# Kernel tuning notes

Hardware: AMD Instinct MI355X
Metric: run time of the kernel (lower is better)

The kernel has to match this reference:

```python
import jax, jax.numpy as jnp
import numpy as np

B = 32768; E = 9; RANK = 50; K = 2
N_ENT = 40943; N_REL = 22
LOSS_COEF = 0.01; NOISE_EPS = 0.01
EPS = float(np.finfo(np.float64).eps)


def setup_inputs():
    key = jax.random.key(0)
    ks = jax.random.split(key, 12)
    q0 = jax.random.randint(ks[0], (B,), 0, N_ENT)
    q1 = jax.random.randint(ks[1], (B,), 0, N_REL)
    q2 = jax.random.randint(ks[2], (B,), 0, N_ENT)
    queries = jnp.stack([q0, q1, q2], axis=1)
    t2 = jax.random.randint(ks[3], (B,), 0, N_ENT)
    these_queries = jnp.stack([q0, q1, t2], axis=1)
    D = E * RANK
    entity = jax.random.normal(ks[4], (N_ENT, D), jnp.float32) / D
    rel = jax.random.normal(ks[5], (N_REL, 2 * D), jnp.float32) / (2 * D)
    rel_diag = 2.0 * jax.random.uniform(ks[6], (N_REL, D), jnp.float32) - 1.0
    bh = jnp.zeros((N_ENT, 1), jnp.float32)
    bt = jnp.zeros((N_ENT, 1), jnp.float32)
    c_param = jnp.ones((N_REL, 1), jnp.float32)
    cnn_w = 0.1 * jax.random.normal(ks[7], (1, 1, 5, 5), jnp.float32)
    cnn_b = jnp.zeros((1,), jnp.float32)
    h2e_w = 0.05 * jax.random.normal(ks[8], (E, 128), jnp.float32)
    h2e_b = jnp.zeros((E,), jnp.float32)
    cnnn_w = 0.1 * jax.random.normal(ks[9], (1, 1, 5, 5), jnp.float32)
    cnnn_b = jnp.zeros((1,), jnp.float32)
    h2en_w = 0.05 * jax.random.normal(ks[10], (E, 128), jnp.float32)
    h2en_b = jnp.zeros((E,), jnp.float32)
    noise = jax.random.normal(ks[11], (B, E), jnp.float32)
    return {"queries": queries, "these_queries": these_queries, "entity": entity,
            "rel": rel, "rel_diag": rel_diag, "bh": bh, "bt": bt, "c_param": c_param,
            "cnn_w": cnn_w, "cnn_b": cnn_b, "h2e_w": h2e_w, "h2e_b": h2e_b,
            "cnnn_w": cnnn_w, "cnnn_b": cnnn_b, "h2en_w": h2en_w, "h2en_b": h2en_b,
            "noise": noise}


def _conv(x, w, b):
    # x: [B,1,27,50], w: [1,1,5,5], stride 3, VALID -> [B,1,8,16]
    y = jax.lax.conv_general_dilated(x, w, (3, 3), 'VALID',
                                     dimension_numbers=('NCHW', 'OIHW', 'NCHW'))
    return y + b.reshape(1, -1, 1, 1)


def _phi(z):
    # standard normal CDF
    return 0.5 * (1.0 + jax.lax.erf(z * 0.7071067811865476))


def _givens_rot(r, x):
    # r, x: [B,E,RANK]; rotate consecutive dim-pairs by normalized (cos,sin) from r
    shp = r.shape[:-1] + (RANK // 2, 2)
    r2 = r.reshape(shp); x2 = x.reshape(shp)
    nrm = jnp.maximum(jnp.linalg.norm(r2, axis=-1, keepdims=True), 1e-15)
    cs = r2 / nrm
    o0 = cs[..., 0] * x2[..., 0] - cs[..., 1] * x2[..., 1]
    o1 = cs[..., 1] * x2[..., 0] + cs[..., 0] * x2[..., 1]
    return jnp.stack([o0, o1], axis=-1).reshape(r.shape)


def _cv_squared(v):
    return jnp.var(v, ddof=1) / (jnp.mean(v) ** 2 + 1e-10)


def reference(queries, these_queries, entity, rel, rel_diag, bh, bt, c_param,
              cnn_w, cnn_b, h2e_w, h2e_b, cnnn_w, cnnn_b, h2en_w, h2en_b, noise):
    q0, q1 = queries[:, 0], queries[:, 1]
    t2 = these_queries[:, 2]
    head = entity[q0]                  # [B, E*RANK]
    rel_q = rel[q1]                    # [B, 2*E*RANK]
    rel_diag_q = rel_diag[q1]          # [B, E*RANK]
    c = jax.nn.softplus(c_param[q1])   # [B, 1]
    lhs_b = bh[q0]                     # [B, 1]
    rhs_b = bt[t2]                     # [B, 1]
    rhs_e = entity[t2]                 # [B, E*RANK]

    # ---- noisy top-k gating ----
    x = jnp.concatenate([head, rel_q], axis=-1).reshape(-1, 1, 3 * E, RANK)
    feat = _conv(x, cnn_w, cnn_b).reshape(-1, 128)
    clean = feat @ h2e_w.T + h2e_b                      # [B, E]
    feat_n = _conv(x, cnnn_w, cnnn_b).reshape(-1, 128)
    raw_std = feat_n @ h2en_w.T + h2en_b
    std = jax.nn.softplus(raw_std) + NOISE_EPS
    noisy = clean + noise * std                         # train=1

    top_logits, top_idx = jax.lax.top_k(noisy, K + 1)
    tk_logits = top_logits[:, :K]
    tk_idx = top_idx[:, :K]
    tk_gates = jax.nn.softmax(tk_logits, axis=-1)
    gates = jnp.zeros_like(noisy).at[jnp.arange(noisy.shape[0])[:, None], tk_idx].set(tk_gates)

    thr_in = top_logits[:, K:K + 1]
    thr_out = top_logits[:, K - 1:K]
    is_in = noisy > thr_in
    prob = jnp.where(is_in, _phi((clean - thr_in) / std), _phi((clean - thr_out) / std))
    load = prob.sum(0)
    importance = gates.sum(0)
    loss = LOSS_COEF * (_cv_squared(importance) + _cv_squared(load))

    # ---- experts, computed densely over [B, E, RANK] then masked-combined ----
    head_r = head.reshape(-1, E, RANK)
    rhs_r = rhs_e.reshape(-1, E, RANK)
    rel_r = rel_q.reshape(-1, E, 2 * RANK)
    rd_r = rel_diag_q.reshape(-1, E, RANK)
    lhs = _givens_rot(rd_r, head_r) + rel_r[..., :RANK]
    dist2 = jnp.sum((lhs - rhs_r) ** 2, axis=-1)        # [B, E]
    score = lhs_b + rhs_b - c * dist2                   # [B, E]

    # SparseDispatcher.combine with use_log_sum_exp=True, multiply_by_gates=False
    mask = gates > 0
    s = jnp.sum(jnp.where(mask, jnp.exp(score), 0.0), axis=1, keepdims=True)
    y = jnp.log(jnp.where(s == 0, EPS, s))              # [B, 1]
    return y, loss
```

## Files before the change

### kernel.cpp

```cpp
#include <hip/hip_runtime.h>
#include <math.h>

#define BATCH 32768
#define NE 9
#define RANK 50
#define DIM 450
#define REL_DIM 900
#define N_REL 22
#define EPSV 2.2204460492503131e-16f
#define SPB 4

#define LANE_FENCE() asm volatile("" ::: "memory")

__device__ __forceinline__ float softplusf(float x) {
    return (x > 20.f) ? x : log1pf(expf(x));
}
__device__ __forceinline__ float phif(float z) {
    return 0.5f * (1.f + erff(z * 0.70710678118654752f));
}

__global__ __launch_bounds__(64) void k_pre(
    const float* __restrict__ rel, const float* __restrict__ rel_diag,
    const float* __restrict__ c_param,
    const float* __restrict__ cnn_w, const float* __restrict__ cnn_b,
    const float* __restrict__ cnnn_w, const float* __restrict__ cnnn_b,
    const float* __restrict__ h2e_w, const float* __restrict__ h2en_w,
    float* __restrict__ cs_tab, float* __restrict__ pre_out, float* __restrict__ c_soft)
{
    const int r = blockIdx.x;
    const int l = threadIdx.x;
    __shared__ float rl[REL_DIM];
    __shared__ float fA[80], fB[80];

    const float* relp = rel + (size_t)r * REL_DIM;
    for (int i = l; i < REL_DIM; i += 64) rl[i] = relp[i];
    __syncthreads();

    const float cb0 = cnn_b[0], cb1 = cnnn_b[0];
    for (int idx = l; idx < 80; idx += 64) {
        int o = 48 + idx;
        int oh = o >> 4, ow = o & 15;
        const float* base = rl + (oh * 3 - 9) * RANK + ow * 3;
        float a0 = cb0, a1 = cb1;
#pragma unroll
        for (int i = 0; i < 5; ++i)
#pragma unroll
            for (int j = 0; j < 5; ++j) {
                float v = base[i * RANK + j];
                a0 = fmaf(v, cnn_w[i * 5 + j], a0);
                a1 = fmaf(v, cnnn_w[i * 5 + j], a1);
            }
        fA[idx] = a0; fB[idx] = a1;
    }
    __syncthreads();

    if (l < 18) {
        int e = (l < 9) ? l : (l - 9);
        const float* w = ((l < 9) ? (h2e_w + e * 128) : (h2en_w + e * 128)) + 48;
        const float* f = (l < 9) ? fA : fB;
        float acc = 0.f;
#pragma unroll 8
        for (int t = 0; t < 80; ++t) acc = fmaf(f[t], w[t], acc);
        pre_out[r * 18 + l] = acc;
    }
    if (l == 63) c_soft[r] = softplusf(c_param[r]);

    const float2* rd2 = (const float2*)(rel_diag + (size_t)r * DIM);
    float2* cs2 = (float2*)(cs_tab + (size_t)r * DIM);
    for (int u = l; u < 225; u += 64) {
        float2 v = rd2[u];
        float nrm = fmaxf(sqrtf(v.x * v.x + v.y * v.y), 1e-15f);
        cs2[u] = make_float2(v.x / nrm, v.y / nrm);
    }
}

__global__ __launch_bounds__(64) void k_main(
    const int* __restrict__ queries, const int* __restrict__ these_queries,
    const float* __restrict__ entity, const float* __restrict__ rel,
    const float* __restrict__ bh, const float* __restrict__ bt,
    const float* __restrict__ cnn_w, const float* __restrict__ cnn_b,
    const float* __restrict__ h2e_w, const float* __restrict__ h2e_b,
    const float* __restrict__ cnnn_w, const float* __restrict__ cnnn_b,
    const float* __restrict__ h2en_w, const float* __restrict__ h2en_b,
    const float* __restrict__ noise,
    const float* __restrict__ cs_tab, const float* __restrict__ pre_out,
    const float* __restrict__ c_soft,
    float* __restrict__ y_out, float* __restrict__ ws_rows)
{
    const int l = threadIdx.x;

    __shared__ __align__(16) float  xs[552];
    __shared__ __align__(16) float2 fs[51];
    float2* xs2 = (float2*)xs;

    const int base = blockIdx.x * SPB;

    int q0 = queries[base * 3 + 0];
    int q1 = queries[base * 3 + 1];
    int t2 = these_queries[base * 3 + 2];
    float2 h2[4];
    {
        const float2* hp2 = (const float2*)(entity + (size_t)q0 * DIM);
#pragma unroll
        for (int k = 0; k < 4; ++k) { int i = l + 64 * k; if (i < 225) h2[k] = hp2[i]; }
    }
    float2 rr2 = make_float2(0.f, 0.f);
    if (l < 50) rr2 = ((const float2*)(rel + (size_t)q1 * REL_DIM))[l];
    float nz    = (l < NE) ? noise[(size_t)base * NE + l] : 0.f;
    float pre_v = (l < 18) ? pre_out[q1 * 18 + l] : 0.f;
    float bhv = bh[q0], btv = bt[t2], csv = c_soft[q1];

#pragma unroll
    for (int s = 0; s < SPB; ++s) {
        const int b = base + s;
        const int   cq1 = q1, ct2 = t2;
        const float cnz = nz, cpre = pre_v, cbh = bhv, cbt = btv, ccs = csv;

#pragma unroll
        for (int k = 0; k < 4; ++k) { int i = l + 64 * k; if (i < 225) xs2[i] = h2[k]; }
        if (l < 50) xs2[225 + l] = rr2;
        LANE_FENCE();

        if (s + 1 < SPB) {
            const int nb = b + 1;
            q0 = queries[nb * 3 + 0];
            q1 = queries[nb * 3 + 1];
            t2 = these_queries[nb * 3 + 2];
            const float2* hp2 = (const float2*)(entity + (size_t)q0 * DIM);
#pragma unroll
            for (int k = 0; k < 4; ++k) { int i = l + 64 * k; if (i < 225) h2[k] = hp2[i]; }
            rr2 = make_float2(0.f, 0.f);
            if (l < 50) rr2 = ((const float2*)(rel + (size_t)q1 * REL_DIM))[l];
            nz    = (l < NE) ? noise[(size_t)nb * NE + l] : 0.f;
            pre_v = (l < 18) ? pre_out[q1 * 18 + l] : 0.f;
            bhv = bh[q0]; btv = bt[t2]; csv = c_soft[q1];
        }

        if (l < 48) {
            int oh = l >> 4, ow = l & 15;
            const float* bp = xs + (oh * 3) * RANK + ow * 3;
            float a0 = cnn_b[0], a1 = cnnn_b[0];
#pragma unroll
            for (int i = 0; i < 5; ++i)
#pragma unroll
                for (int j = 0; j < 5; ++j) {
                    float v = bp[i * RANK + j];
                    a0 = fmaf(v, cnn_w[i * 5 + j], a0);
                    a1 = fmaf(v, cnnn_w[i * 5 + j], a1);
                }
            fs[l + (l >> 4)] = make_float2(a0, a1);
        }
        LANE_FENCE();

        float acc = 0.f;
        if (l < 54) {
            int chunk = l / 18, j = l - chunk * 18;
            int e = (j < 9) ? j : (j - 9);
            const float* wrow = ((j < 9) ? (h2e_w + e * 128) : (h2en_w + e * 128)) + chunk * 16;
            int fbase = chunk * 17;
            if (j < 9) {
#pragma unroll
                for (int k = 0; k < 16; ++k) acc = fmaf(fs[fbase + k].x, wrow[k], acc);
            } else {
#pragma unroll
                for (int k = 0; k < 16; ++k) acc = fmaf(fs[fbase + k].y, wrow[k], acc);
            }
        }
        float pA = __shfl_down(acc, 18);
        float pB = __shfl_down(acc, 36);
        float tot = acc + pA + pB;

        float myv = 0.f;
        if (l < 9)       myv = tot + cpre + h2e_b[l];
        else if (l < 18) myv = softplusf(tot + cpre + h2en_b[l - 9]) + 0.01f;
        float sd = __shfl_down(myv, 9);
        float nv = fmaf(cnz, sd, myv);

        int i0 = -1, i1 = -1;
        float v0 = -__builtin_huge_valf(), v1 = v0, v2 = v0;
#pragma unroll
        for (int e = 0; e < NE; ++e) {
            float v = __shfl(nv, e);
            if (v > v0)      { v2 = v1; v1 = v0; i1 = i0; v0 = v; i0 = e; }
            else if (v > v1) { v2 = v1; v1 = v; i1 = e; }
            else if (v > v2) { v2 = v; }
        }
        float e1 = expf(v1 - v0);
        float inv = 1.f / (1.f + e1);
        float g0 = inv, g1 = e1 * inv;
        float thr_in = v2, thr_out = v1;

        int srcl = (l >= 9 && l < 18) ? (l - 9) : 0;
        float cl_e = __shfl(myv, srcl);
        float nv_e = __shfl(nv, srcl);

        float contrib = 0.f;
        bool act = (l < 25) || (l >= 32 && l < 57);
        if (act) {
            int sel = (l >= 32) ? 1 : 0;
            int p = l - 32 * sel;
            int e = sel ? i1 : i0;
            int u = e * 25 + p;
            float2 cs = *(const float2*)(cs_tab + (size_t)cq1 * DIM + 2 * u);
            float2 rl = *(const float2*)(rel + (size_t)cq1 * REL_DIM + e * 100 + 2 * p);
            float2 rh = *(const float2*)(entity + (size_t)ct2 * DIM + 2 * u);
            float2 x  = xs2[u];
            float o0 = cs.x * x.x - cs.y * x.y + rl.x;
            float o1 = cs.y * x.x + cs.x * x.y + rl.y;
            float d0 = o0 - rh.x, d1 = o1 - rh.y;
            contrib = fmaf(d0, d0, d1 * d1);
        }

        if (l < NE) {
            float g = (l == i0) ? g0 : ((l == i1) ? g1 : 0.f);
            ws_rows[(size_t)b * 18 + l] = g;
        } else if (l < 18) {
            float thr = (nv_e > thr_in) ? thr_in : thr_out;
            ws_rows[(size_t)b * 18 + l] = phif((cl_e - thr) / myv);
        }

#pragma unroll
        for (int off = 16; off; off >>= 1) contrib += __shfl_xor(contrib, off);
        float d2b = __shfl(contrib, 32);
        if (l == 0) {
            float bsum = cbh + cbt;
            float sacc = expf(bsum - ccs * contrib) + expf(bsum - ccs * d2b);
            y_out[b] = logf((sacc == 0.f) ? EPSV : sacc);
        }
        LANE_FENCE();
    }
}

__global__ __launch_bounds__(64) void k_reduce(const float* __restrict__ ws_rows,
                                               float* __restrict__ partials)
{
    const int blk = blockIdx.x, t = threadIdx.x;
    float acc[18];
#pragma unroll
    for (int j = 0; j < 18; ++j) acc[j] = 0.f;
    const int r0 = blk * 128 + t * 2;
#pragma unroll
    for (int rr = 0; rr < 2; ++rr) {
        const float2* row = (const float2*)(ws_rows + (size_t)(r0 + rr) * 18);
#pragma unroll
        for (int j = 0; j < 9; ++j) {
            float2 v = row[j];
            acc[2 * j] += v.x; acc[2 * j + 1] += v.y;
        }
    }
#pragma unroll
    for (int j = 0; j < 18; ++j) {
        float v = acc[j];
        for (int off = 32; off; off >>= 1) v += __shfl_down(v, off);
        if (t == 0) partials[blk * 18 + j] = v;
    }
}

__global__ __launch_bounds__(64) void k_loss(const float* __restrict__ partials,
                                             float* __restrict__ out)
{
    __shared__ float sums[18];
    const int t = threadIdx.x;
    if (t < 18) {
        float s = 0.f;
        for (int p0 = 0; p0 < 256; p0 += 16) {
            float v[16];
#pragma unroll
            for (int k = 0; k < 16; ++k) v[k] = partials[(p0 + k) * 18 + t];
#pragma unroll
            for (int k = 0; k < 16; ++k) s += v[k];
        }
        sums[t] = s;
    }
    __syncthreads();
    if (t == 0) {
        float loss = 0.f;
#pragma unroll
        for (int part = 0; part < 2; ++part) {
            const float* v = sums + part * NE;
            float mean = 0.f;
            for (int i = 0; i < NE; ++i) mean += v[i];
            mean /= 9.f;
            float var = 0.f;
            for (int i = 0; i < NE; ++i) { float d = v[i] - mean; var += d * d; }
            var /= 8.f;
            loss += var / (mean * mean + 1e-10f);
        }
        out[BATCH] = 0.01f * loss;
    }
}

extern "C" void kernel_launch(void* const* d_in, const int* in_sizes, int n_in,
                              void* d_out, int out_size, void* d_ws, size_t ws_size,
                              hipStream_t stream)
{
    const int*   queries = (const int*)d_in[0];
    const int*   these   = (const int*)d_in[1];
    const float* entity  = (const float*)d_in[2];
    const float* rel     = (const float*)d_in[3];
    const float* rel_dg  = (const float*)d_in[4];
    const float* bh      = (const float*)d_in[5];
    const float* bt      = (const float*)d_in[6];
    const float* c_par   = (const float*)d_in[7];
    const float* cnn_w   = (const float*)d_in[8];
    const float* cnn_b   = (const float*)d_in[9];
    const float* h2e_w   = (const float*)d_in[10];
    const float* h2e_b   = (const float*)d_in[11];
    const float* cnnn_w  = (const float*)d_in[12];
    const float* cnnn_b  = (const float*)d_in[13];
    const float* h2en_w  = (const float*)d_in[14];
    const float* h2en_b  = (const float*)d_in[15];
    const float* noise   = (const float*)d_in[16];

    float* y  = (float*)d_out;
    float* ws = (float*)d_ws;
    float* ws_rows  = ws;
    float* partials = ws + (size_t)BATCH * 18;
    float* cs_tab   = partials + 256 * 18;
    float* pre_out  = cs_tab + N_REL * DIM;
    float* c_soft   = pre_out + N_REL * 18;

    k_pre<<<N_REL, 64, 0, stream>>>(rel, rel_dg, c_par, cnn_w, cnn_b, cnnn_w, cnnn_b,
                                    h2e_w, h2en_w, cs_tab, pre_out, c_soft);
    k_main<<<BATCH / SPB, 64, 0, stream>>>(queries, these, entity, rel, bh, bt,
                                           cnn_w, cnn_b, h2e_w, h2e_b, cnnn_w, cnnn_b,
                                           h2en_w, h2en_b, noise, cs_tab, pre_out, c_soft,
                                           y, ws_rows);
    k_reduce<<<256, 64, 0, stream>>>(ws_rows, partials);
    k_loss<<<1, 64, 0, stream>>>(partials, y);
}
```

Measured before the change: 193.7 us.

## Process one sample per block instead of four with software prefetch

Removes the four-samples-per-block loop and its software prefetch of the next sample's entity row and relation data, launching one 64-thread block per batch element. Query indices are made wave-uniform with readfirstlane so the gathered row addresses can stay in scalar registers. The aim is more independent blocks to hide gather latency through occupancy instead of in-block prefetch. The cost is four times as many blocks and more per-block setup, including repeated loads of the small weight vectors.

```diff
diff --git a/kernel.cpp b/kernel.cpp
--- a/kernel.cpp
+++ b/kernel.cpp
@@ -8,7 +8,6 @@
 #define REL_DIM 900
 #define N_REL 22
 #define EPSV 2.2204460492503131e-16f
-#define SPB 4
 
 #define LANE_FENCE() asm volatile("" ::: "memory")
 
@@ -87,17 +86,17 @@
     const float* __restrict__ c_soft,
     float* __restrict__ y_out, float* __restrict__ ws_rows)
 {
+    const int b = blockIdx.x;
     const int l = threadIdx.x;
 
     __shared__ __align__(16) float  xs[552];
     __shared__ __align__(16) float2 fs[51];
     float2* xs2 = (float2*)xs;
 
-    const int base = blockIdx.x * SPB;
-
-    int q0 = queries[base * 3 + 0];
-    int q1 = queries[base * 3 + 1];
-    int t2 = these_queries[base * 3 + 2];
+    const int q0 = __builtin_amdgcn_readfirstlane(queries[b * 3 + 0]);
+    const int q1 = __builtin_amdgcn_readfirstlane(queries[b * 3 + 1]);
+    const int t2 = __builtin_amdgcn_readfirstlane(these_queries[b * 3 + 2]);
+
     float2 h2[4];
     {
         const float2* hp2 = (const float2*)(entity + (size_t)q0 * DIM);
@@ -106,128 +105,105 @@
     }
     float2 rr2 = make_float2(0.f, 0.f);
     if (l < 50) rr2 = ((const float2*)(rel + (size_t)q1 * REL_DIM))[l];
-    float nz    = (l < NE) ? noise[(size_t)base * NE + l] : 0.f;
+    float nz    = (l < NE) ? noise[(size_t)b * NE + l] : 0.f;
     float pre_v = (l < 18) ? pre_out[q1 * 18 + l] : 0.f;
     float bhv = bh[q0], btv = bt[t2], csv = c_soft[q1];
 
 #pragma unroll
-    for (int s = 0; s < SPB; ++s) {
-        const int b = base + s;
-        const int   cq1 = q1, ct2 = t2;
-        const float cnz = nz, cpre = pre_v, cbh = bhv, cbt = btv, ccs = csv;
-
-#pragma unroll
-        for (int k = 0; k < 4; ++k) { int i = l + 64 * k; if (i < 225) xs2[i] = h2[k]; }
-        if (l < 50) xs2[225 + l] = rr2;
-        LANE_FENCE();
-
-        if (s + 1 < SPB) {
-            const int nb = b + 1;
-            q0 = queries[nb * 3 + 0];
-            q1 = queries[nb * 3 + 1];
-            t2 = these_queries[nb * 3 + 2];
-            const float2* hp2 = (const float2*)(entity + (size_t)q0 * DIM);
-#pragma unroll
-            for (int k = 0; k < 4; ++k) { int i = l + 64 * k; if (i < 225) h2[k] = hp2[i]; }
-            rr2 = make_float2(0.f, 0.f);
-            if (l < 50) rr2 = ((const float2*)(rel + (size_t)q1 * REL_DIM))[l];
-            nz    = (l < NE) ? noise[(size_t)nb * NE + l] : 0.f;
-            pre_v = (l < 18) ? pre_out[q1 * 18 + l] : 0.f;
-            bhv = bh[q0]; btv = bt[t2]; csv = c_soft[q1];
+    for (int k = 0; k < 4; ++k) { int i = l + 64 * k; if (i < 225) xs2[i] = h2[k]; }
+    if (l < 50) xs2[225 + l] = rr2;
+    LANE_FENCE();
+
+    if (l < 48) {
+        int oh = l >> 4, ow = l & 15;
+        const float* bp = xs + (oh * 3) * RANK + ow * 3;
+        float a0 = cnn_b[0], a1 = cnnn_b[0];
+#pragma unroll
+        for (int i = 0; i < 5; ++i)
+#pragma unroll
+            for (int j = 0; j < 5; ++j) {
+                float v = bp[i * RANK + j];
+                a0 = fmaf(v, cnn_w[i * 5 + j], a0);
+                a1 = fmaf(v, cnnn_w[i * 5 + j], a1);
+            }
+        fs[l + (l >> 4)] = make_float2(a0, a1);
+    }
+    LANE_FENCE();
+
+    float acc = 0.f;
+    if (l < 54) {
+        int chunk = l / 18, j = l - chunk * 18;
+        int e = (j < 9) ? j : (j - 9);
+        const float* wrow = ((j < 9) ? (h2e_w + e * 128) : (h2en_w + e * 128)) + chunk * 16;
+        int fbase = chunk * 17;
+        if (j < 9) {
+#pragma unroll
+            for (int k = 0; k < 16; ++k) acc = fmaf(fs[fbase + k].x, wrow[k], acc);
+        } else {
+#pragma unroll
+            for (int k = 0; k < 16; ++k) acc = fmaf(fs[fbase + k].y, wrow[k], acc);
         }
-
-        if (l < 48) {
-            int oh = l >> 4, ow = l & 15;
-            const float* bp = xs + (oh * 3) * RANK + ow * 3;
-            float a0 = cnn_b[0], a1 = cnnn_b[0];
-#pragma unroll
-            for (int i = 0; i < 5; ++i)
-#pragma unroll
-                for (int j = 0; j < 5; ++j) {
-                    float v = bp[i * RANK + j];
-                    a0 = fmaf(v, cnn_w[i * 5 + j], a0);
-                    a1 = fmaf(v, cnnn_w[i * 5 + j], a1);
-                }
-            fs[l + (l >> 4)] = make_float2(a0, a1);
-        }
-        LANE_FENCE();
-
-        float acc = 0.f;
-        if (l < 54) {
-            int chunk = l / 18, j = l - chunk * 18;
-            int e = (j < 9) ? j : (j - 9);
-            const float* wrow = ((j < 9) ? (h2e_w + e * 128) : (h2en_w + e * 128)) + chunk * 16;
-            int fbase = chunk * 17;
-            if (j < 9) {
-#pragma unroll
-                for (int k = 0; k < 16; ++k) acc = fmaf(fs[fbase + k].x, wrow[k], acc);
-            } else {
-#pragma unroll
-                for (int k = 0; k < 16; ++k) acc = fmaf(fs[fbase + k].y, wrow[k], acc);
-            }
-        }
-        float pA = __shfl_down(acc, 18);
-        float pB = __shfl_down(acc, 36);
-        float tot = acc + pA + pB;
-
-        float myv = 0.f;
-        if (l < 9)       myv = tot + cpre + h2e_b[l];
-        else if (l < 18) myv = softplusf(tot + cpre + h2en_b[l - 9]) + 0.01f;
-        float sd = __shfl_down(myv, 9);
-        float nv = fmaf(cnz, sd, myv);
-
-        int i0 = -1, i1 = -1;
-        float v0 = -__builtin_huge_valf(), v1 = v0, v2 = v0;
-#pragma unroll
-        for (int e = 0; e < NE; ++e) {
-            float v = __shfl(nv, e);
-            if (v > v0)      { v2 = v1; v1 = v0; i1 = i0; v0 = v; i0 = e; }
-            else if (v > v1) { v2 = v1; v1 = v; i1 = e; }
-            else if (v > v2) { v2 = v; }
-        }
-        float e1 = expf(v1 - v0);
-        float inv = 1.f / (1.f + e1);
-        float g0 = inv, g1 = e1 * inv;
-        float thr_in = v2, thr_out = v1;
-
-        int srcl = (l >= 9 && l < 18) ? (l - 9) : 0;
-        float cl_e = __shfl(myv, srcl);
-        float nv_e = __shfl(nv, srcl);
-
-        float contrib = 0.f;
-        bool act = (l < 25) || (l >= 32 && l < 57);
-        if (act) {
-            int sel = (l >= 32) ? 1 : 0;
-            int p = l - 32 * sel;
-            int e = sel ? i1 : i0;
-            int u = e * 25 + p;
-            float2 cs = *(const float2*)(cs_tab + (size_t)cq1 * DIM + 2 * u);
-            float2 rl = *(const float2*)(rel + (size_t)cq1 * REL_DIM + e * 100 + 2 * p);
-            float2 rh = *(const float2*)(entity + (size_t)ct2 * DIM + 2 * u);
-            float2 x  = xs2[u];
-            float o0 = cs.x * x.x - cs.y * x.y + rl.x;
-            float o1 = cs.y * x.x + cs.x * x.y + rl.y;
-            float d0 = o0 - rh.x, d1 = o1 - rh.y;
-            contrib = fmaf(d0, d0, d1 * d1);
-        }
-
-        if (l < NE) {
-            float g = (l == i0) ? g0 : ((l == i1) ? g1 : 0.f);
-            ws_rows[(size_t)b * 18 + l] = g;
-        } else if (l < 18) {
-            float thr = (nv_e > thr_in) ? thr_in : thr_out;
-            ws_rows[(size_t)b * 18 + l] = phif((cl_e - thr) / myv);
-        }
-
-#pragma unroll
-        for (int off = 16; off; off >>= 1) contrib += __shfl_xor(contrib, off);
-        float d2b = __shfl(contrib, 32);
-        if (l == 0) {
-            float bsum = cbh + cbt;
-            float sacc = expf(bsum - ccs * contrib) + expf(bsum - ccs * d2b);
-            y_out[b] = logf((sacc == 0.f) ? EPSV : sacc);
-        }
-        LANE_FENCE();
+    }
+    float pA = __shfl_down(acc, 18);
+    float pB = __shfl_down(acc, 36);
+    float tot = acc + pA + pB;
+
+    float myv = 0.f;
+    if (l < 9)       myv = tot + pre_v + h2e_b[l];
+    else if (l < 18) myv = softplusf(tot + pre_v + h2en_b[l - 9]) + 0.01f;
+    float sd = __shfl_down(myv, 9);
+    float nv = fmaf(nz, sd, myv);
+
+    int i0 = -1, i1 = -1;
+    float v0 = -__builtin_huge_valf(), v1 = v0, v2 = v0;
+#pragma unroll
+    for (int e = 0; e < NE; ++e) {
+        float v = __shfl(nv, e);
+        if (v > v0)      { v2 = v1; v1 = v0; i1 = i0; v0 = v; i0 = e; }
+        else if (v > v1) { v2 = v1; v1 = v; i1 = e; }
+        else if (v > v2) { v2 = v; }
+    }
+    float e1 = expf(v1 - v0);
+    float inv = 1.f / (1.f + e1);
+    float g0 = inv, g1 = e1 * inv;
+    float thr_in = v2, thr_out = v1;
+
+    int srcl = (l >= 9 && l < 18) ? (l - 9) : 0;
+    float cl_e = __shfl(myv, srcl);
+    float nv_e = __shfl(nv, srcl);
+
+    float contrib = 0.f;
+    bool act = (l < 25) || (l >= 32 && l < 57);
+    if (act) {
+        int sel = (l >= 32) ? 1 : 0;
+        int p = l - 32 * sel;
+        int e = sel ? i1 : i0;
+        int u = e * 25 + p;
+        float2 cs = *(const float2*)(cs_tab + (size_t)q1 * DIM + 2 * u);
+        float2 rl = *(const float2*)(rel + (size_t)q1 * REL_DIM + e * 100 + 2 * p);
+        float2 rh = *(const float2*)(entity + (size_t)t2 * DIM + 2 * u);
+        float2 x  = xs2[u];
+        float o0 = cs.x * x.x - cs.y * x.y + rl.x;
+        float o1 = cs.y * x.x + cs.x * x.y + rl.y;
+        float d0 = o0 - rh.x, d1 = o1 - rh.y;
+        contrib = fmaf(d0, d0, d1 * d1);
+    }
+
+    if (l < NE) {
+        float g = (l == i0) ? g0 : ((l == i1) ? g1 : 0.f);
+        ws_rows[(size_t)b * 18 + l] = g;
+    } else if (l < 18) {
+        float thr = (nv_e > thr_in) ? thr_in : thr_out;
+        ws_rows[(size_t)b * 18 + l] = phif((cl_e - thr) / myv);
+    }
+
+#pragma unroll
+    for (int off = 16; off; off >>= 1) contrib += __shfl_xor(contrib, off);
+    float d2b = __shfl(contrib, 32);
+    if (l == 0) {
+        float bsum = bhv + btv;
+        float sacc = expf(bsum - csv * contrib) + expf(bsum - csv * d2b);
+        y_out[b] = logf((sacc == 0.f) ? EPSV : sacc);
     }
 }
 
@@ -322,10 +298,10 @@
 
     k_pre<<<N_REL, 64, 0, stream>>>(rel, rel_dg, c_par, cnn_w, cnn_b, cnnn_w, cnnn_b,
                                     h2e_w, h2en_w, cs_tab, pre_out, c_soft);
-    k_main<<<BATCH / SPB, 64, 0, stream>>>(queries, these, entity, rel, bh, bt,
-                                           cnn_w, cnn_b, h2e_w, h2e_b, cnnn_w, cnnn_b,
-                                           h2en_w, h2en_b, noise, cs_tab, pre_out, c_soft,
-                                           y, ws_rows);
+    k_main<<<BATCH, 64, 0, stream>>>(queries, these, entity, rel, bh, bt,
+                                     cnn_w, cnn_b, h2e_w, h2e_b, cnnn_w, cnnn_b,
+                                     h2en_w, h2en_b, noise, cs_tab, pre_out, c_soft,
+                                     y, ws_rows);
     k_reduce<<<256, 64, 0, stream>>>(ws_rows, partials);
     k_loss<<<1, 64, 0, stream>>>(partials, y);
 }
```

Measured after the change: 184.1 us. -5.0%, faster.
